# Performance work log

Measured on AMD Instinct MI355X. Metric: run time of the kernel, lower is better.

## Reference

```python
import jax, jax.numpy as jnp
import numpy as np

N_NODES = 50000
N_EVENTS = 500000
P = 127          # previous_embed_size
A = P + 1        # agg_features
O = A + P        # w2 out size = 255
BN_EPS = 1e-5


def setup_inputs() -> dict:
    key = jax.random.key(0)
    ks = jax.random.split(key, 12)
    inp = {
        "u": jax.random.randint(ks[0], (N_EVENTS,), 0, N_NODES),
        "v": jax.random.randint(ks[1], (N_EVENTS,), 0, N_NODES),
        "g": jax.random.uniform(ks[2], (N_EVENTS, 1), dtype=jnp.float32),
        "h": jax.random.normal(ks[3], (N_NODES, P), dtype=jnp.float32),
        "remember_u": jax.random.normal(ks[4], (N_EVENTS, P), dtype=jnp.float32),
        "remember_v": jax.random.normal(ks[5], (N_EVENTS, P), dtype=jnp.float32),
        "bn_gamma": jnp.ones((A,), jnp.float32),
        "bn_beta": jnp.zeros((A,), jnp.float32),
        "w1_w": jax.random.normal(ks[6], (A, A), dtype=jnp.float32) / np.sqrt(A),
        "w1_b": jax.random.normal(ks[7], (A,), dtype=jnp.float32) * 0.01,
        "w2_w": jax.random.normal(ks[8], (O, O), dtype=jnp.float32) / np.sqrt(O),
        "w2_b": jax.random.normal(ks[9], (O,), dtype=jnp.float32) * 0.01,
        "event": N_EVENTS,
    }
    return inp


def reference(u, v, g, h, remember_u, remember_v, bn_gamma, bn_beta,
              w1_w, w1_b, w2_w, w2_b, event):
    n_nodes = h.shape[0]
    agg_feat = bn_gamma.shape[0]
    # per-edge messages: cat(stale embedding, time feature)  -> [E, A]
    src_u = jnp.concatenate([remember_u, g], axis=1)
    src_v = jnp.concatenate([remember_v, g], axis=1)
    # scatter_add into node buffers (row-wise scatter, index expanded in torch)
    agg_v = jnp.zeros((n_nodes, agg_feat), g.dtype).at[v].add(src_u)
    agg_u = jnp.zeros((n_nodes, agg_feat), g.dtype).at[u].add(src_v)
    agg = agg_u + agg_v  # [N, A]
    # BatchNorm1d (training mode: batch stats over node dim, biased var)
    mean = jnp.mean(agg, axis=0)
    var = jnp.var(agg, axis=0)
    x = (agg - mean) * jax.lax.rsqrt(var + BN_EPS) * bn_gamma + bn_beta
    # 2-layer MLP with skip-cat of h
    x1 = jax.nn.relu(x @ w1_w.T + w1_b)                 # [N, A]
    out = jnp.concatenate([h, x1], axis=1) @ w2_w.T + w2_b  # [N, A+P]
    return out
```

## Files before the change

kernel.cpp:

```cpp
#include <hip/hip_runtime.h>

constexpr int PDIM = 127;
constexpr int ADIM = 128;
constexpr int ODIM = 255;
constexpr int RTILE = 32;
constexpr int CAP = 80;
constexpr float EPS = 1e-5f;

constexpr int XS_STRIDE = 136;
constexpr int CS_STRIDE = 264;

typedef short bf16x8 __attribute__((ext_vector_type(8)));
typedef float f32x4 __attribute__((ext_vector_type(4)));

__device__ inline unsigned short f2b(float x) {
    unsigned u = __builtin_bit_cast(unsigned, x);
    u += 0x7FFF + ((u >> 16) & 1);
    return (unsigned short)(u >> 16);
}

__global__ __launch_bounds__(256) void bucket_kernel(
    const int* __restrict__ u, const int* __restrict__ v,
    int* __restrict__ cnt, int* __restrict__ bucket, int E)
{
    int e = blockIdx.x * 256 + threadIdx.x;
    if (e >= E) return;
    int vn = v[e];
    int slot = atomicAdd(&cnt[vn], 1);
    if (slot < CAP) bucket[(long long)vn * CAP + slot] = e;
    int un = u[e];
    slot = atomicAdd(&cnt[un], 1);
    if (slot < CAP) bucket[(long long)un * CAP + slot] = e | (1 << 20);
}

__global__ __launch_bounds__(256) void gather_kernel(
    const int* __restrict__ cnt, const int* __restrict__ bucket,
    const float* __restrict__ g,
    const float* __restrict__ ru, const float* __restrict__ rv,
    float* __restrict__ agg, int N)
{
    int wid0 = (blockIdx.x * 256 + threadIdx.x) >> 6;
    if (wid0 >= N) return;
    int wid = __builtin_amdgcn_readfirstlane(wid0);
    int lane = threadIdx.x & 63;
    int deg = cnt[wid];
    if (deg > CAP) deg = CAP;
    const int* bkt = bucket + (long long)wid * CAP;
    int cA = (lane < deg) ? bkt[lane] : 0;
    int cB = (lane + 64 < deg) ? bkt[lane + 64] : 0;

    float a0 = 0.f, a1 = 0.f;
    bool lo = (lane < 63);

    int d = 0;
    for (; d + 8 <= deg; d += 8) {
        float x0[8], x1[8];
        #pragma unroll
        for (int k = 0; k < 8; ++k) {
            int dd = d + k;
            int c = (dd < 64) ? __builtin_amdgcn_readlane(cA, dd)
                              : __builtin_amdgcn_readlane(cB, dd - 64);
            int e = c & 0xFFFFF;
            const float* s = (c & (1 << 20)) ? rv : ru;
            long long B = (long long)e * PDIM;
            const float* p1 = lo ? (s + B + 64 + lane) : (g + e);
            x0[k] = s[B + lane];
            x1[k] = *p1;
        }
        #pragma unroll
        for (int k = 0; k < 8; ++k) { a0 += x0[k]; a1 += x1[k]; }
    }
    for (; d < deg; ++d) {
        int c = (d < 64) ? __builtin_amdgcn_readlane(cA, d)
                         : __builtin_amdgcn_readlane(cB, d - 64);
        int e = c & 0xFFFFF;
        const float* s = (c & (1 << 20)) ? rv : ru;
        long long B = (long long)e * PDIM;
        const float* p1 = lo ? (s + B + 64 + lane) : (g + e);
        a0 += s[B + lane];
        a1 += *p1;
    }
    agg[(long long)wid * ADIM + lane] = a0;
    agg[(long long)wid * ADIM + 64 + lane] = a1;
}

__global__ __launch_bounds__(256) void colstats_kernel(
    const float* __restrict__ agg, float* __restrict__ csum,
    float* __restrict__ csumsq, int N)
{
    int j = threadIdx.x & 127;
    int rh = threadIdx.x >> 7;
    float s = 0.f, ss = 0.f;
    for (int r = blockIdx.x * 2 + rh; r < N; r += gridDim.x * 2) {
        float x = agg[(long long)r * ADIM + j];
        s += x; ss += x * x;
    }
    __shared__ float sh[2][128];
    __shared__ float sh2[2][128];
    sh[rh][j] = s; sh2[rh][j] = ss;
    __syncthreads();
    if (threadIdx.x < 128) {
        unsafeAtomicAdd(&csum[j], sh[0][j] + sh[1][j]);
        unsafeAtomicAdd(&csumsq[j], sh2[0][j] + sh2[1][j]);
    }
}

__global__ void finalize_kernel(const float* __restrict__ csum,
                                const float* __restrict__ csumsq,
                                const float* __restrict__ gamma,
                                const float* __restrict__ beta,
                                float* __restrict__ scale,
                                float* __restrict__ shift, int N)
{
    int j = threadIdx.x;
    if (j >= ADIM) return;
    float inv = 1.f / (float)N;
    float mean = csum[j] * inv;
    float var = csumsq[j] * inv - mean * mean;
    float sc = gamma[j] * rsqrtf(var + EPS);
    scale[j] = sc;
    shift[j] = beta[j] - mean * sc;
}

__global__ __launch_bounds__(256) void wprep_kernel(
    const float* __restrict__ w1, const float* __restrict__ w2,
    unsigned short* __restrict__ w1b, unsigned short* __restrict__ w2b)
{
    int t = blockIdx.x * 256 + threadIdx.x;
    if (t < 65536) {
        int o = t >> 8, k = t & 255;
        w2b[t] = (o < ODIM && k < ODIM) ? f2b(w2[o * ODIM + k]) : (unsigned short)0;
    } else {
        int s = t - 65536;
        if (s < ADIM * ADIM) w1b[s] = f2b(w1[s]);
    }
}

__global__ __launch_bounds__(256, 4) void mlp_kernel(
    const float* __restrict__ agg, const float* __restrict__ h,
    const float* __restrict__ scale, const float* __restrict__ shift,
    const unsigned short* __restrict__ w1b, const float* __restrict__ b1,
    const unsigned short* __restrict__ w2b, const float* __restrict__ b2,
    float* __restrict__ out, int N)
{
    __shared__ unsigned short xs[RTILE * XS_STRIDE];
    __shared__ unsigned short cs[RTILE * CS_STRIDE];
    int tid = threadIdx.x;
    int row0 = blockIdx.x * RTILE;
    int lane = tid & 63;
    int wave = tid >> 6;

    {
        int j = tid & 127, rh = tid >> 7;
        float sc = scale[j], sf = shift[j];
        for (int i = 0; i < RTILE / 2; ++i) {
            int r = i * 2 + rh;
            long long grow = row0 + r;
            float x = 0.f, hv = 0.f;
            if (grow < N) {
                x = agg[grow * ADIM + j] * sc + sf;
                if (j < PDIM) hv = h[grow * PDIM + j];
            }
            xs[r * XS_STRIDE + j] = f2b(x);
            cs[r * CS_STRIDE + j] = f2b(hv);
        }
        if (tid < RTILE) cs[tid * CS_STRIDE + 255] = 0;
    }
    __syncthreads();

    {
        int arow = lane & 15, akg = lane >> 4;
        bf16x8 afr[2][4];
        #pragma unroll
        for (int rt = 0; rt < 2; ++rt)
            #pragma unroll
            for (int ks = 0; ks < 4; ++ks)
                afr[rt][ks] = *reinterpret_cast<const bf16x8*>(
                    &xs[(rt * 16 + arow) * XS_STRIDE + ks * 32 + akg * 8]);
        #pragma unroll
        for (int t = 0; t < 2; ++t) {
            int bcol = (wave * 2 + t) * 16 + (lane & 15);
            bf16x8 bfr[4];
            #pragma unroll
            for (int ks = 0; ks < 4; ++ks)
                bfr[ks] = *reinterpret_cast<const bf16x8*>(&w1b[bcol * ADIM + ks * 32 + akg * 8]);
            float bias = b1[bcol];
            #pragma unroll
            for (int rt = 0; rt < 2; ++rt) {
                f32x4 acc = {0.f, 0.f, 0.f, 0.f};
                #pragma unroll
                for (int ks = 0; ks < 4; ++ks)
                    acc = __builtin_amdgcn_mfma_f32_16x16x32_bf16(afr[rt][ks], bfr[ks], acc, 0, 0, 0);
                #pragma unroll
                for (int i = 0; i < 4; ++i) {
                    int r = rt * 16 + (lane >> 4) * 4 + i;
                    float x1 = fmaxf(acc[i] + bias, 0.f);
                    cs[r * CS_STRIDE + PDIM + bcol] = f2b(x1);
                }
            }
        }
    }
    __syncthreads();

    {
        int arow = lane & 15, akg = lane >> 4;
        bf16x8 caf[2][8];
        #pragma unroll
        for (int rt = 0; rt < 2; ++rt)
            #pragma unroll
            for (int ks = 0; ks < 8; ++ks)
                caf[rt][ks] = *reinterpret_cast<const bf16x8*>(
                    &cs[(rt * 16 + arow) * CS_STRIDE + ks * 32 + akg * 8]);
        #pragma unroll
        for (int t = 0; t < 4; ++t) {
            int o = (wave * 4 + t) * 16 + (lane & 15);
            bf16x8 bfr[8];
            #pragma unroll
            for (int ks = 0; ks < 8; ++ks)
                bfr[ks] = *reinterpret_cast<const bf16x8*>(&w2b[o * 256 + ks * 32 + akg * 8]);
            float bias = (o < ODIM) ? b2[o] : 0.f;
            #pragma unroll
            for (int rt = 0; rt < 2; ++rt) {
                f32x4 acc = {0.f, 0.f, 0.f, 0.f};
                #pragma unroll
                for (int ks = 0; ks < 8; ++ks)
                    acc = __builtin_amdgcn_mfma_f32_16x16x32_bf16(caf[rt][ks], bfr[ks], acc, 0, 0, 0);
                if (o < ODIM) {
                    #pragma unroll
                    for (int i = 0; i < 4; ++i) {
                        long long grow = row0 + rt * 16 + (lane >> 4) * 4 + i;
                        if (grow < N) out[grow * ODIM + o] = acc[i] + bias;
                    }
                }
            }
        }
    }
}

extern "C" void kernel_launch(void* const* d_in, const int* in_sizes, int n_in,
                              void* d_out, int out_size, void* d_ws, size_t ws_size,
                              hipStream_t stream)
{
    const int*   u     = (const int*)d_in[0];
    const int*   v     = (const int*)d_in[1];
    const float* g     = (const float*)d_in[2];
    const float* h     = (const float*)d_in[3];
    const float* ru    = (const float*)d_in[4];
    const float* rv    = (const float*)d_in[5];
    const float* gamma = (const float*)d_in[6];
    const float* beta  = (const float*)d_in[7];
    const float* w1w   = (const float*)d_in[8];
    const float* w1b_f = (const float*)d_in[9];
    const float* w2w   = (const float*)d_in[10];
    const float* w2b_f = (const float*)d_in[11];

    int E = in_sizes[0];
    int N = in_sizes[3] / PDIM;

    int*   cnt    = (int*)d_ws;
    float* csum   = (float*)d_ws + N;
    float* csumsq = csum + ADIM;
    float* scale  = csumsq + ADIM;
    float* shift  = scale + ADIM;
    int*   bucket = (int*)(shift + ADIM);
    float* agg    = (float*)(bucket + (long long)N * CAP);
    unsigned short* w1b = (unsigned short*)(agg + (long long)N * ADIM);
    unsigned short* w2b = w1b + ADIM * ADIM;

    (void)hipMemsetAsync(cnt, 0, ((size_t)N + 2 * ADIM) * sizeof(float), stream);

    wprep_kernel<<<(65536 + ADIM * ADIM + 255) / 256, 256, 0, stream>>>(w1w, w2w, w1b, w2b);

    bucket_kernel<<<(E + 255) / 256, 256, 0, stream>>>(u, v, cnt, bucket, E);

    long long gthreads = (long long)N * 64;
    gather_kernel<<<(int)((gthreads + 255) / 256), 256, 0, stream>>>(
        cnt, bucket, g, ru, rv, agg, N);

    colstats_kernel<<<1024, 256, 0, stream>>>(agg, csum, csumsq, N);
    finalize_kernel<<<1, 128, 0, stream>>>(csum, csumsq, gamma, beta, scale, shift, N);

    int mblocks = (N + RTILE - 1) / RTILE;
    mlp_kernel<<<mblocks, 256, 0, stream>>>(agg, h, scale, shift, w1b, w1b_f, w2b, w2b_f,
                                            (float*)d_out, N);
}
```

Baseline: 304.1 us.

## Vectorize gather with half-wave per node and pre-sum time feature via atomics

```diff
diff --git a/kernel.cpp b/kernel.cpp
--- a/kernel.cpp
+++ b/kernel.cpp
@@ -21,67 +21,72 @@
 
 __global__ __launch_bounds__(256) void bucket_kernel(
     const int* __restrict__ u, const int* __restrict__ v,
-    int* __restrict__ cnt, int* __restrict__ bucket, int E)
+    const float* __restrict__ g,
+    int* __restrict__ cnt, int* __restrict__ bucket,
+    float* __restrict__ gsum, int E)
 {
     int e = blockIdx.x * 256 + threadIdx.x;
     if (e >= E) return;
+    float gv = g[e];
     int vn = v[e];
     int slot = atomicAdd(&cnt[vn], 1);
     if (slot < CAP) bucket[(long long)vn * CAP + slot] = e;
+    unsafeAtomicAdd(&gsum[vn], gv);
     int un = u[e];
     slot = atomicAdd(&cnt[un], 1);
     if (slot < CAP) bucket[(long long)un * CAP + slot] = e | (1 << 20);
+    unsafeAtomicAdd(&gsum[un], gv);
 }
 
 __global__ __launch_bounds__(256) void gather_kernel(
     const int* __restrict__ cnt, const int* __restrict__ bucket,
-    const float* __restrict__ g,
+    const float* __restrict__ gsum,
     const float* __restrict__ ru, const float* __restrict__ rv,
     float* __restrict__ agg, int N)
 {
-    int wid0 = (blockIdx.x * 256 + threadIdx.x) >> 6;
-    if (wid0 >= N) return;
-    int wid = __builtin_amdgcn_readfirstlane(wid0);
-    int lane = threadIdx.x & 63;
-    int deg = cnt[wid];
+    __shared__ int codes[8][CAP];
+    int tid = threadIdx.x;
+    int hw = tid >> 5;
+    int sub = tid & 31;
+    long long node = (long long)blockIdx.x * 8 + hw;
+    bool valid = (node < N);
+    int nd = valid ? (int)node : 0;
+    int deg = valid ? cnt[nd] : 0;
     if (deg > CAP) deg = CAP;
-    const int* bkt = bucket + (long long)wid * CAP;
-    int cA = (lane < deg) ? bkt[lane] : 0;
-    int cB = (lane + 64 < deg) ? bkt[lane + 64] : 0;
-
-    float a0 = 0.f, a1 = 0.f;
-    bool lo = (lane < 63);
-
+    const int* bkt = bucket + (long long)nd * CAP;
+    codes[hw][sub] = bkt[sub];
+    codes[hw][32 + sub] = bkt[32 + sub];
+    if (sub < CAP - 64) codes[hw][64 + sub] = bkt[64 + sub];
+
+    int eoff = (sub < 31) ? 4 * sub : 123;
+    f32x4 acc = {0.f, 0.f, 0.f, 0.f};
     int d = 0;
-    for (; d + 8 <= deg; d += 8) {
-        float x0[8], x1[8];
-        #pragma unroll
-        for (int k = 0; k < 8; ++k) {
-            int dd = d + k;
-            int c = (dd < 64) ? __builtin_amdgcn_readlane(cA, dd)
-                              : __builtin_amdgcn_readlane(cB, dd - 64);
+    for (; d + 4 <= deg; d += 4) {
+        f32x4 vb[4];
+        #pragma unroll
+        for (int k = 0; k < 4; ++k) {
+            int c = codes[hw][d + k];
             int e = c & 0xFFFFF;
             const float* s = (c & (1 << 20)) ? rv : ru;
-            long long B = (long long)e * PDIM;
-            const float* p1 = lo ? (s + B + 64 + lane) : (g + e);
-            x0[k] = s[B + lane];
-            x1[k] = *p1;
-        }
-        #pragma unroll
-        for (int k = 0; k < 8; ++k) { a0 += x0[k]; a1 += x1[k]; }
+            vb[k] = *reinterpret_cast<const f32x4*>(s + (long long)e * PDIM + eoff);
+        }
+        #pragma unroll
+        for (int k = 0; k < 4; ++k) acc += vb[k];
     }
     for (; d < deg; ++d) {
-        int c = (d < 64) ? __builtin_amdgcn_readlane(cA, d)
-                         : __builtin_amdgcn_readlane(cB, d - 64);
+        int c = codes[hw][d];
         int e = c & 0xFFFFF;
         const float* s = (c & (1 << 20)) ? rv : ru;
-        long long B = (long long)e * PDIM;
-        const float* p1 = lo ? (s + B + 64 + lane) : (g + e);
-        a0 += s[B + lane];
-        a1 += *p1;
-    }
-    agg[(long long)wid * ADIM + lane] = a0;
-    agg[(long long)wid * ADIM + 64 + lane] = a1;
+        acc += *reinterpret_cast<const f32x4*>(s + (long long)e * PDIM + eoff);
+    }
+    if (!valid) return;
+    float* arow = agg + node * ADIM;
+    if (sub < 31) {
+        *reinterpret_cast<f32x4*>(arow + 4 * sub) = acc;
+    } else {
+        f32x4 o; o.x = acc.y; o.y = acc.z; o.z = acc.w; o.w = gsum[nd];
+        *reinterpret_cast<f32x4*>(arow + 124) = o;
+    }
 }
 
 __global__ __launch_bounds__(256) void colstats_kernel(
@@ -258,7 +263,8 @@
     int N = in_sizes[3] / PDIM;
 
     int*   cnt    = (int*)d_ws;
-    float* csum   = (float*)d_ws + N;
+    float* gsum   = (float*)d_ws + N;
+    float* csum   = gsum + N;
     float* csumsq = csum + ADIM;
     float* scale  = csumsq + ADIM;
     float* shift  = scale + ADIM;
@@ -267,15 +273,14 @@
     unsigned short* w1b = (unsigned short*)(agg + (long long)N * ADIM);
     unsigned short* w2b = w1b + ADIM * ADIM;
 
-    (void)hipMemsetAsync(cnt, 0, ((size_t)N + 2 * ADIM) * sizeof(float), stream);
+    (void)hipMemsetAsync(cnt, 0, ((size_t)(2 * N) + 2 * ADIM) * sizeof(float), stream);
 
     wprep_kernel<<<(65536 + ADIM * ADIM + 255) / 256, 256, 0, stream>>>(w1w, w2w, w1b, w2b);
 
-    bucket_kernel<<<(E + 255) / 256, 256, 0, stream>>>(u, v, cnt, bucket, E);
-
-    long long gthreads = (long long)N * 64;
-    gather_kernel<<<(int)((gthreads + 255) / 256), 256, 0, stream>>>(
-        cnt, bucket, g, ru, rv, agg, N);
+    bucket_kernel<<<(E + 255) / 256, 256, 0, stream>>>(u, v, g, cnt, bucket, gsum, E);
+
+    int gblocks = (N + 7) / 8;
+    gather_kernel<<<gblocks, 256, 0, stream>>>(cnt, bucket, gsum, ru, rv, agg, N);
 
     colstats_kernel<<<1024, 256, 0, stream>>>(agg, csum, csumsq, N);
     finalize_kernel<<<1, 128, 0, stream>>>(csum, csumsq, gamma, beta, scale, shift, N);
```

Result: slower. 326.4 us (+7.3%).
